# Optimization experiments

Measured on AMD Instinct MI355X. Metric: run time of the kernel, lower is better.

Reference implementation:

```python
import jax, jax.numpy as jnp
import numpy as np

ASSIGN_RATIO = 0.1  # hard-coded inside coarsen_graph in the original
EPS_CUT = 1e-7
EPS_NORM = 1e-12  # torch F.normalize eps


def _normalize_batch_adj(adj):
    # adj: [B, N, N]
    n = adj.shape[1]
    A = adj + jnp.eye(n, dtype=adj.dtype)
    deg_inv_sqrt = jnp.clip(A.sum(-1), 1.0, None) ** -0.5  # [B, N]
    newA = deg_inv_sqrt[..., :, None] * A * deg_inv_sqrt[..., None, :]
    row_mask = (adj.sum(-1) > 0).astype(adj.dtype)  # [B, N]
    return row_mask[..., :, None] * newA


def setup_inputs():
    key = jax.random.key(0)
    k0, k1, k2, k3, k4 = jax.random.split(key, 5)
    B, N, D, T = 512, 128, 256, 512
    concept_hidden = jax.random.normal(k0, (B, N, D), jnp.float32)
    adj = jax.random.uniform(k1, (B, N, N), jnp.float32)
    head = jax.random.randint(k2, (B, T), 0, N)
    lin_w = jax.random.normal(k3, (1, D), jnp.float32) / np.sqrt(D).astype(np.float32)
    bias = jax.random.normal(k4, (1,), jnp.float32)
    return {"concept_hidden": concept_hidden, "adj": adj, "head": head,
            "lin_w": lin_w, "bias": bias}


def reference(concept_hidden, adj, head, lin_w, bias):
    # concept_hidden: [B, N, D], adj: [B, N, N], head: [B, T] node indices
    x = concept_hidden
    B, N, D = x.shape

    out = x @ lin_w.T                      # [B, N, 1]  self.lin(x)
    norm_adj = _normalize_batch_adj(adj)   # [B, N, N]
    out = norm_adj @ out + bias            # [B, N, 1]
    alpha = jax.nn.sigmoid(out ** 2)[..., 0]  # [B, N]

    # batch_num_nodes[i] = len(set(head[i]))  -> count unique via sort
    hs = jnp.sort(head, axis=-1)
    n_uniq = 1 + (hs[:, 1:] != hs[:, :-1]).sum(-1)  # [B]

    # per-sample k = ceil(n * 0.1) + 1 (only when n > 1); cut = k-th largest alpha
    k = jnp.ceil(n_uniq.astype(jnp.float32) * ASSIGN_RATIO).astype(jnp.int32) + 1
    a_desc = jnp.sort(alpha, axis=-1)[:, ::-1]       # descending
    idx = jnp.clip(k - 1, 0, N - 1)
    cut = jnp.take_along_axis(a_desc, idx[:, None], axis=-1)[:, 0]
    cut = jnp.where(n_uniq > 1, cut, jnp.zeros_like(cut))  # [B]

    cut_alpha = jax.nn.relu(alpha + EPS_CUT - cut[:, None])  # [B, N]

    # S = norm_adj * cut_alpha broadcast over rows, then L1-normalize rows
    S = norm_adj * cut_alpha[:, None, :]
    S = S / jnp.clip(jnp.abs(S).sum(-1, keepdims=True), EPS_NORM, None)

    St = jnp.swapaxes(S, 1, 2)             # [B, N, N]
    embedding_tensor = St @ x              # S^T x   [B, N, D]
    new_adj = (St @ adj) @ S               # S^T A S [B, N, N]
    return embedding_tensor, new_adj
```

## Files before the change

kernel.cpp:

```cpp
#include <hip/hip_runtime.h>

#define Bsz 512
#define Nn  128
#define Dd  256
#define Tt  512

typedef __attribute__((ext_vector_type(8))) short short8;
typedef __attribute__((ext_vector_type(4))) float f32x4;

__device__ __forceinline__ ushort f2bf(float f) {
    union { float f; unsigned u; } v; v.f = f;
    unsigned r = v.u + 0x7fffu + ((v.u >> 16) & 1u);
    return (ushort)(r >> 16);
}
__device__ __forceinline__ unsigned pk2(float a, float b) {
    return (unsigned)f2bf(a) | ((unsigned)f2bf(b) << 16);
}
__device__ __forceinline__ float bf2f(ushort u) {
    union { unsigned u; float f; } v; v.u = (unsigned)u << 16; return v.f;
}

__global__ __launch_bounds__(1024, 8) void mega(
    const float* __restrict__ x, const float* __restrict__ adj,
    const int* __restrict__ head, const float* __restrict__ lin_w,
    const float* __restrict__ bias,
    float* __restrict__ emb, float* __restrict__ nadj)
{
    const int b = blockIdx.x, t = threadIdx.x;
    __shared__ __align__(16) ushort adjB[Nn][136];
    __shared__ __align__(16) ushort STl[Nn][136];
    __shared__ float ttS[Nn], disS[Nn], maskS[Nn], alphaS[Nn], uS[Nn], rowcS[Nn];
    __shared__ float partS[Nn][9];
    __shared__ float dotP[Nn][4];
    __shared__ int   flags[Nn];
    __shared__ int   nuniq;
    __shared__ float cutS;

    const float bias0 = bias[0];
    if (t < Nn) flags[t] = 0;
    if (t == 0) { nuniq = 0; cutS = 0.f; }

    const float* adjb = adj + (size_t)b * Nn * Nn;
#pragma unroll
    for (int i = 0; i < 4; ++i) {
        int f = t + 1024 * i;
        int rr = f >> 5, c = (f & 31) * 4;
        float4 v = *(const float4*)&adjb[(size_t)rr * Nn + c];
        uint2 w2; w2.x = pk2(v.x, v.y); w2.y = pk2(v.z, v.w);
        *(uint2*)&adjB[rr][c] = w2;
    }
    __syncthreads();

    if (t < Tt) { int h = head[(size_t)b * Tt + t]; flags[h] = 1; }

    if (t < 512) {
        const int dr = t >> 2, dh = t & 3;
        const float4* xr = (const float4*)(x + ((size_t)b * Nn + dr) * Dd + dh * 64);
        const float4* wr = (const float4*)(lin_w + dh * 64);
        float p = 0.f;
#pragma unroll
        for (int i = 0; i < 16; ++i) {
            float4 v = xr[i], w4 = wr[i];
            p += v.x * w4.x + v.y * w4.y + v.z * w4.z + v.w * w4.w;
        }
        dotP[dr][dh] = p;
    }

    const int r = t >> 3, seg = t & 7;
    {
        short8 a0 = *(const short8*)&adjB[r][seg * 16];
        short8 a1 = *(const short8*)&adjB[r][seg * 16 + 8];
        float s = 0.f;
#pragma unroll
        for (int j = 0; j < 8; ++j) s += bf2f((ushort)a0[j]) + bf2f((ushort)a1[j]);
        partS[r][seg] = s;
    }
    __syncthreads();

    if (t < Nn) {
        float rs = 0.f;
#pragma unroll
        for (int j = 0; j < 8; ++j) rs += partS[t][j];
        float dt = dotP[t][0] + dotP[t][1] + dotP[t][2] + dotP[t][3];
        maskS[t]  = (rs > 0.f) ? 1.f : 0.f;
        float dis = 1.f / sqrtf(fmaxf(rs + 1.f, 1.f));
        disS[t]   = dis;
        ttS[t]    = dis * dt;
        atomicAdd(&nuniq, flags[t]);
    }
    __syncthreads();

    {
        short8 a0 = *(const short8*)&adjB[r][seg * 16];
        short8 a1 = *(const short8*)&adjB[r][seg * 16 + 8];
        float s = 0.f;
#pragma unroll
        for (int j = 0; j < 8; ++j) {
            s += bf2f((ushort)a0[j]) * ttS[seg * 16 + j];
            s += bf2f((ushort)a1[j]) * ttS[seg * 16 + 8 + j];
        }
        partS[r][seg] = s;
    }
    __syncthreads();
    if (t < Nn) {
        float mv = 0.f;
#pragma unroll
        for (int j = 0; j < 8; ++j) mv += partS[t][j];
        float o = maskS[t] * disS[t] * (mv + ttS[t]) + bias0;
        alphaS[t] = 1.f / (1.f + expf(-o * o));
    }
    __syncthreads();
    if (t < Nn) {
        int nu = nuniq;
        if (nu > 1) {
            int idx = (int)ceilf((float)nu * 0.1f);
            if (idx > Nn - 1) idx = Nn - 1;
            float an = alphaS[t];
            int cg = 0, ce = 0;
            for (int j = 0; j < Nn; ++j) {
                float aj = alphaS[j];
                cg += (aj > an); ce += (aj == an);
            }
            if (cg <= idx && idx < cg + ce) cutS = an;
        }
    }
    __syncthreads();
    if (t < Nn) uS[t] = fmaxf(alphaS[t] + 1e-7f - cutS, 0.f) * disS[t];
    __syncthreads();
    {
        short8 a0 = *(const short8*)&adjB[r][seg * 16];
        short8 a1 = *(const short8*)&adjB[r][seg * 16 + 8];
        float s = 0.f;
#pragma unroll
        for (int j = 0; j < 8; ++j) {
            s += bf2f((ushort)a0[j]) * uS[seg * 16 + j];
            s += bf2f((ushort)a1[j]) * uS[seg * 16 + 8 + j];
        }
        partS[r][seg] = s;
    }
    __syncthreads();
    if (t < Nn) {
        float tot = uS[t];
#pragma unroll
        for (int j = 0; j < 8; ++j) tot += partS[t][j];
        float rsum = maskS[t] * disS[t] * tot;
        rowcS[t]   = maskS[t] * disS[t] / fmaxf(rsum, 1e-12f);
    }
    __syncthreads();

    {
        const int m = t & 127, sl = t >> 7, k0 = sl * 16;
        const float um = uS[m];
        float vv[16];
#pragma unroll
        for (int j = 0; j < 16; ++j) {
            int k = k0 + j;
            vv[j] = rowcS[k] * (bf2f(adjB[k][m]) + ((k == m) ? 1.f : 0.f)) * um;
        }
        uint4 p0, p1;
        p0.x = pk2(vv[0],  vv[1]);  p0.y = pk2(vv[2],  vv[3]);
        p0.z = pk2(vv[4],  vv[5]);  p0.w = pk2(vv[6],  vv[7]);
        p1.x = pk2(vv[8],  vv[9]);  p1.y = pk2(vv[10], vv[11]);
        p1.z = pk2(vv[12], vv[13]); p1.w = pk2(vv[14], vv[15]);
        *(uint4*)&STl[m][k0]     = p0;
        *(uint4*)&STl[m][k0 + 8] = p1;
    }
    __syncthreads();

    const int lane = t & 63, w = t >> 6;
    const int l15 = lane & 15, quad = lane >> 4;
    const int mrow  = (w & 7) * 16;
    const int nhalf = (w >> 3) * 64;
    f32x4 acc[4];

#pragma unroll
    for (int nt = 0; nt < 4; ++nt) acc[nt] = (f32x4){0.f, 0.f, 0.f, 0.f};
#pragma unroll
    for (int k0 = 0; k0 < 128; k0 += 32) {
        short8 a0 = *(const short8*)&adjB[mrow + l15][k0 + quad * 8];
#pragma unroll
        for (int nt = 0; nt < 4; ++nt) {
            short8 bf = *(const short8*)&STl[nhalf + nt * 16 + l15][k0 + quad * 8];
            acc[nt] = __builtin_amdgcn_mfma_f32_16x16x32_bf16(a0, bf, acc[nt], 0, 0, 0);
        }
    }
    __syncthreads();

    ushort (*PT)[136] = (ushort(*)[136])&adjB[0][0];
#pragma unroll
    for (int nt = 0; nt < 4; ++nt) {
        int j    = nhalf + nt * 16 + l15;
        int mcol = mrow + quad * 4;
        uint2 w2;
        w2.x = pk2(acc[nt][0], acc[nt][1]);
        w2.y = pk2(acc[nt][2], acc[nt][3]);
        *(uint2*)&PT[j][mcol] = w2;
    }
    __syncthreads();

#pragma unroll
    for (int nt = 0; nt < 4; ++nt) acc[nt] = (f32x4){0.f, 0.f, 0.f, 0.f};
#pragma unroll
    for (int k0 = 0; k0 < 128; k0 += 32) {
        short8 a0 = *(const short8*)&STl[mrow + l15][k0 + quad * 8];
#pragma unroll
        for (int nt = 0; nt < 4; ++nt) {
            short8 bf = *(const short8*)&PT[nhalf + nt * 16 + l15][k0 + quad * 8];
            acc[nt] = __builtin_amdgcn_mfma_f32_16x16x32_bf16(a0, bf, acc[nt], 0, 0, 0);
        }
    }
#pragma unroll
    for (int nt = 0; nt < 4; ++nt)
#pragma unroll
        for (int rr = 0; rr < 4; ++rr) {
            int row = mrow + quad * 4 + rr;
            int col = nhalf + nt * 16 + l15;
            nadj[((size_t)b * Nn + row) * Nn + col] = acc[nt][rr];
        }
    __syncthreads();

    uint (*xTp)[68] = (uint(*)[68])&adjB[0][0];
    short8 aE[4];
#pragma unroll
    for (int ks = 0; ks < 4; ++ks)
        aE[ks] = *(const short8*)&STl[mrow + l15][ks * 32 + quad * 8];
    const int dcb = (w >> 3) * 64;

    for (int half = 0; half < 2; ++half) {
        const int d0 = half * 128;
#pragma unroll
        for (int i = 0; i < 2; ++i) {
            int f = t + 1024 * i;
            int d4 = f & 31, kp = f >> 5;
            const float* xp = x + ((size_t)b * Nn + 2 * kp) * Dd + d0 + 4 * d4;
            float4 ve = *(const float4*)xp;
            float4 vo = *(const float4*)(xp + Dd);
            xTp[4 * d4    ][kp] = pk2(ve.x, vo.x);
            xTp[4 * d4 + 1][kp] = pk2(ve.y, vo.y);
            xTp[4 * d4 + 2][kp] = pk2(ve.z, vo.z);
            xTp[4 * d4 + 3][kp] = pk2(ve.w, vo.w);
        }
        __syncthreads();
        f32x4 accE[4];
#pragma unroll
        for (int nt = 0; nt < 4; ++nt) accE[nt] = (f32x4){0.f, 0.f, 0.f, 0.f};
#pragma unroll
        for (int ks = 0; ks < 4; ++ks) {
#pragma unroll
            for (int nt = 0; nt < 4; ++nt) {
                short8 bf = *(const short8*)&xTp[dcb + nt * 16 + l15][ks * 16 + quad * 4];
                accE[nt] = __builtin_amdgcn_mfma_f32_16x16x32_bf16(aE[ks], bf, accE[nt], 0, 0, 0);
            }
        }
#pragma unroll
        for (int nt = 0; nt < 4; ++nt)
#pragma unroll
            for (int rr = 0; rr < 4; ++rr) {
                int row = mrow + quad * 4 + rr;
                int col = d0 + dcb + nt * 16 + l15;
                emb[((size_t)b * Nn + row) * Dd + col] = accE[nt][rr];
            }
        __syncthreads();
    }
}

extern "C" void kernel_launch(void* const* d_in, const int* in_sizes, int n_in,
                              void* d_out, int out_size, void* d_ws, size_t ws_size,
                              hipStream_t stream)
{
    const float* x     = (const float*)d_in[0];
    const float* adj   = (const float*)d_in[1];
    const int*   head  = (const int*)d_in[2];
    const float* lin_w = (const float*)d_in[3];
    const float* bias  = (const float*)d_in[4];

    float* emb  = (float*)d_out;
    float* nadj = emb + (size_t)Bsz * Nn * Dd;

    mega<<<Bsz, 1024, 0, stream>>>(x, adj, head, lin_w, bias, emb, nadj);
}
```

Measured before the change: 199.7 us.

## Overlap adj load with dot products, shuffle reductions, prefetch x into registers

The first phase is split so half the threads compute the x·w dot products while the other half load and convert adj to bf16. The shared-memory partial-sum arrays and their extra barriers are replaced by wavefront shuffle reductions. The x tiles for the embedding GEMM are loaded into registers before the second adjacency GEMM and before the first embedding half, hiding global latency behind MFMA work. In exchange it uses more registers and issues strided scalar x loads instead of float4 loads.

After: 198.9 us. About the same (-0.4%).

```diff
diff --git a/kernel.cpp b/kernel.cpp
--- a/kernel.cpp
+++ b/kernel.cpp
@@ -30,8 +30,7 @@
     __shared__ __align__(16) ushort adjB[Nn][136];
     __shared__ __align__(16) ushort STl[Nn][136];
     __shared__ float ttS[Nn], disS[Nn], maskS[Nn], alphaS[Nn], uS[Nn], rowcS[Nn];
-    __shared__ float partS[Nn][9];
-    __shared__ float dotP[Nn][4];
+    __shared__ float dotL[Nn];
     __shared__ int   flags[Nn];
     __shared__ int   nuniq;
     __shared__ float cutS;
@@ -40,20 +39,9 @@
     if (t < Nn) flags[t] = 0;
     if (t == 0) { nuniq = 0; cutS = 0.f; }
 
-    const float* adjb = adj + (size_t)b * Nn * Nn;
-#pragma unroll
-    for (int i = 0; i < 4; ++i) {
-        int f = t + 1024 * i;
-        int rr = f >> 5, c = (f & 31) * 4;
-        float4 v = *(const float4*)&adjb[(size_t)rr * Nn + c];
-        uint2 w2; w2.x = pk2(v.x, v.y); w2.y = pk2(v.z, v.w);
-        *(uint2*)&adjB[rr][c] = w2;
-    }
-    __syncthreads();
-
-    if (t < Tt) { int h = head[(size_t)b * Tt + t]; flags[h] = 1; }
-
+    int hv = 0;
     if (t < 512) {
+        hv = head[(size_t)b * Tt + t];
         const int dr = t >> 2, dh = t & 3;
         const float4* xr = (const float4*)(x + ((size_t)b * Nn + dr) * Dd + dh * 64);
         const float4* wr = (const float4*)(lin_w + dh * 64);
@@ -63,8 +51,24 @@
             float4 v = xr[i], w4 = wr[i];
             p += v.x * w4.x + v.y * w4.y + v.z * w4.z + v.w * w4.w;
         }
-        dotP[dr][dh] = p;
-    }
+        p += __shfl_xor(p, 1, 64);
+        p += __shfl_xor(p, 2, 64);
+        if (dh == 0) dotL[dr] = p;
+    } else {
+        const int t2 = t - 512;
+        const float* adjb = adj + (size_t)b * Nn * Nn;
+#pragma unroll
+        for (int i = 0; i < 8; ++i) {
+            int f = t2 + 512 * i;
+            int rr = f >> 5, c = (f & 31) * 4;
+            float4 v = *(const float4*)&adjb[(size_t)rr * Nn + c];
+            uint2 w2; w2.x = pk2(v.x, v.y); w2.y = pk2(v.z, v.w);
+            *(uint2*)&adjB[rr][c] = w2;
+        }
+    }
+    __syncthreads();
+
+    if (t < Tt) flags[hv] = 1;
 
     const int r = t >> 3, seg = t & 7;
     {
@@ -73,20 +77,15 @@
         float s = 0.f;
 #pragma unroll
         for (int j = 0; j < 8; ++j) s += bf2f((ushort)a0[j]) + bf2f((ushort)a1[j]);
-        partS[r][seg] = s;
-    }
-    __syncthreads();
-
-    if (t < Nn) {
-        float rs = 0.f;
-#pragma unroll
-        for (int j = 0; j < 8; ++j) rs += partS[t][j];
-        float dt = dotP[t][0] + dotP[t][1] + dotP[t][2] + dotP[t][3];
-        maskS[t]  = (rs > 0.f) ? 1.f : 0.f;
-        float dis = 1.f / sqrtf(fmaxf(rs + 1.f, 1.f));
-        disS[t]   = dis;
-        ttS[t]    = dis * dt;
-        atomicAdd(&nuniq, flags[t]);
+        s += __shfl_xor(s, 1, 64);
+        s += __shfl_xor(s, 2, 64);
+        s += __shfl_xor(s, 4, 64);
+        if (seg == 0) {
+            maskS[r] = (s > 0.f) ? 1.f : 0.f;
+            float dis = 1.f / sqrtf(fmaxf(s + 1.f, 1.f));
+            disS[r] = dis;
+            ttS[r]  = dis * dotL[r];
+        }
     }
     __syncthreads();
 
@@ -99,17 +98,17 @@
             s += bf2f((ushort)a0[j]) * ttS[seg * 16 + j];
             s += bf2f((ushort)a1[j]) * ttS[seg * 16 + 8 + j];
         }
-        partS[r][seg] = s;
-    }
-    __syncthreads();
-    if (t < Nn) {
-        float mv = 0.f;
-#pragma unroll
-        for (int j = 0; j < 8; ++j) mv += partS[t][j];
-        float o = maskS[t] * disS[t] * (mv + ttS[t]) + bias0;
-        alphaS[t] = 1.f / (1.f + expf(-o * o));
-    }
-    __syncthreads();
+        s += __shfl_xor(s, 1, 64);
+        s += __shfl_xor(s, 2, 64);
+        s += __shfl_xor(s, 4, 64);
+        if (seg == 0) {
+            float o = maskS[r] * disS[r] * (s + ttS[r]) + bias0;
+            alphaS[r] = 1.f / (1.f + expf(-o * o));
+            atomicAdd(&nuniq, flags[r]);
+        }
+    }
+    __syncthreads();
+
     if (t < Nn) {
         int nu = nuniq;
         if (nu > 1) {
@@ -127,6 +126,7 @@
     __syncthreads();
     if (t < Nn) uS[t] = fmaxf(alphaS[t] + 1e-7f - cutS, 0.f) * disS[t];
     __syncthreads();
+
     {
         short8 a0 = *(const short8*)&adjB[r][seg * 16];
         short8 a1 = *(const short8*)&adjB[r][seg * 16 + 8];
@@ -136,15 +136,13 @@
             s += bf2f((ushort)a0[j]) * uS[seg * 16 + j];
             s += bf2f((ushort)a1[j]) * uS[seg * 16 + 8 + j];
         }
-        partS[r][seg] = s;
-    }
-    __syncthreads();
-    if (t < Nn) {
-        float tot = uS[t];
-#pragma unroll
-        for (int j = 0; j < 8; ++j) tot += partS[t][j];
-        float rsum = maskS[t] * disS[t] * tot;
-        rowcS[t]   = maskS[t] * disS[t] / fmaxf(rsum, 1e-12f);
+        s += __shfl_xor(s, 1, 64);
+        s += __shfl_xor(s, 2, 64);
+        s += __shfl_xor(s, 4, 64);
+        if (seg == 0) {
+            float rsum = maskS[r] * disS[r] * (uS[r] + s);
+            rowcS[r]   = maskS[r] * disS[r] / fmaxf(rsum, 1e-12f);
+        }
     }
     __syncthreads();
 
@@ -198,6 +196,16 @@
     }
     __syncthreads();
 
+    const int xrow = t & 127, kq0 = t >> 7;
+    float xv0[8], xv1[8];
+    {
+        const float* xb = x + (size_t)b * Nn * Dd + xrow;
+#pragma unroll
+        for (int k = 0; k < 8; ++k) xv0[k] = xb[(size_t)(8 * kq0 + k) * Dd];
+#pragma unroll
+        for (int k = 0; k < 8; ++k) xv1[k] = xb[(size_t)(8 * (kq0 + 8) + k) * Dd];
+    }
+
 #pragma unroll
     for (int nt = 0; nt < 4; ++nt) acc[nt] = (f32x4){0.f, 0.f, 0.f, 0.f};
 #pragma unroll
@@ -212,56 +220,87 @@
 #pragma unroll
     for (int nt = 0; nt < 4; ++nt)
 #pragma unroll
-        for (int rr = 0; rr < 4; ++rr) {
-            int row = mrow + quad * 4 + rr;
+        for (int rr2 = 0; rr2 < 4; ++rr2) {
+            int row = mrow + quad * 4 + rr2;
             int col = nhalf + nt * 16 + l15;
-            nadj[((size_t)b * Nn + row) * Nn + col] = acc[nt][rr];
+            nadj[((size_t)b * Nn + row) * Nn + col] = acc[nt][rr2];
         }
     __syncthreads();
 
     uint (*xTp)[68] = (uint(*)[68])&adjB[0][0];
-    short8 aE[4];
-#pragma unroll
-    for (int ks = 0; ks < 4; ++ks)
-        aE[ks] = *(const short8*)&STl[mrow + l15][ks * 32 + quad * 8];
     const int dcb = (w >> 3) * 64;
 
-    for (int half = 0; half < 2; ++half) {
-        const int d0 = half * 128;
-#pragma unroll
-        for (int i = 0; i < 2; ++i) {
-            int f = t + 1024 * i;
-            int d4 = f & 31, kp = f >> 5;
-            const float* xp = x + ((size_t)b * Nn + 2 * kp) * Dd + d0 + 4 * d4;
-            float4 ve = *(const float4*)xp;
-            float4 vo = *(const float4*)(xp + Dd);
-            xTp[4 * d4    ][kp] = pk2(ve.x, vo.x);
-            xTp[4 * d4 + 1][kp] = pk2(ve.y, vo.y);
-            xTp[4 * d4 + 2][kp] = pk2(ve.z, vo.z);
-            xTp[4 * d4 + 3][kp] = pk2(ve.w, vo.w);
-        }
-        __syncthreads();
-        f32x4 accE[4];
-#pragma unroll
-        for (int nt = 0; nt < 4; ++nt) accE[nt] = (f32x4){0.f, 0.f, 0.f, 0.f};
-#pragma unroll
-        for (int ks = 0; ks < 4; ++ks) {
-#pragma unroll
-            for (int nt = 0; nt < 4; ++nt) {
-                short8 bf = *(const short8*)&xTp[dcb + nt * 16 + l15][ks * 16 + quad * 4];
-                accE[nt] = __builtin_amdgcn_mfma_f32_16x16x32_bf16(aE[ks], bf, accE[nt], 0, 0, 0);
-            }
-        }
-#pragma unroll
-        for (int nt = 0; nt < 4; ++nt)
-#pragma unroll
-            for (int rr = 0; rr < 4; ++rr) {
-                int row = mrow + quad * 4 + rr;
-                int col = d0 + dcb + nt * 16 + l15;
-                emb[((size_t)b * Nn + row) * Dd + col] = accE[nt][rr];
-            }
-        __syncthreads();
-    }
+    {
+        uint4 q;
+        q.x = pk2(xv0[0], xv0[1]); q.y = pk2(xv0[2], xv0[3]);
+        q.z = pk2(xv0[4], xv0[5]); q.w = pk2(xv0[6], xv0[7]);
+        *(uint4*)&xTp[xrow][4 * kq0] = q;
+        q.x = pk2(xv1[0], xv1[1]); q.y = pk2(xv1[2], xv1[3]);
+        q.z = pk2(xv1[4], xv1[5]); q.w = pk2(xv1[6], xv1[7]);
+        *(uint4*)&xTp[xrow][4 * (kq0 + 8)] = q;
+    }
+    __syncthreads();
+
+    {
+        const float* xb = x + (size_t)b * Nn * Dd + 128 + xrow;
+#pragma unroll
+        for (int k = 0; k < 8; ++k) xv0[k] = xb[(size_t)(8 * kq0 + k) * Dd];
+#pragma unroll
+        for (int k = 0; k < 8; ++k) xv1[k] = xb[(size_t)(8 * (kq0 + 8) + k) * Dd];
+    }
+
+    f32x4 accE[4];
+#pragma unroll
+    for (int nt = 0; nt < 4; ++nt) accE[nt] = (f32x4){0.f, 0.f, 0.f, 0.f};
+#pragma unroll
+    for (int ks = 0; ks < 4; ++ks) {
+        short8 aE = *(const short8*)&STl[mrow + l15][ks * 32 + quad * 8];
+#pragma unroll
+        for (int nt = 0; nt < 4; ++nt) {
+            short8 bf = *(const short8*)&xTp[dcb + nt * 16 + l15][ks * 16 + quad * 4];
+            accE[nt] = __builtin_amdgcn_mfma_f32_16x16x32_bf16(aE, bf, accE[nt], 0, 0, 0);
+        }
+    }
+#pragma unroll
+    for (int nt = 0; nt < 4; ++nt)
+#pragma unroll
+        for (int rr2 = 0; rr2 < 4; ++rr2) {
+            int row = mrow + quad * 4 + rr2;
+            int col = dcb + nt * 16 + l15;
+            emb[((size_t)b * Nn + row) * Dd + col] = accE[nt][rr2];
+        }
+    __syncthreads();
+
+    {
+        uint4 q;
+        q.x = pk2(xv0[0], xv0[1]); q.y = pk2(xv0[2], xv0[3]);
+        q.z = pk2(xv0[4], xv0[5]); q.w = pk2(xv0[6], xv0[7]);
+        *(uint4*)&xTp[xrow][4 * kq0] = q;
+        q.x = pk2(xv1[0], xv1[1]); q.y = pk2(xv1[2], xv1[3]);
+        q.z = pk2(xv1[4], xv1[5]); q.w = pk2(xv1[6], xv1[7]);
+        *(uint4*)&xTp[xrow][4 * (kq0 + 8)] = q;
+    }
+    __syncthreads();
+
+#pragma unroll
+    for (int nt = 0; nt < 4; ++nt) accE[nt] = (f32x4){0.f, 0.f, 0.f, 0.f};
+#pragma unroll
+    for (int ks = 0; ks < 4; ++ks) {
+        short8 aE = *(const short8*)&STl[mrow + l15][ks * 32 + quad * 8];
+#pragma unroll
+        for (int nt = 0; nt < 4; ++nt) {
+            short8 bf = *(const short8*)&xTp[dcb + nt * 16 + l15][ks * 16 + quad * 4];
+            accE[nt] = __builtin_amdgcn_mfma_f32_16x16x32_bf16(aE, bf, accE[nt], 0, 0, 0);
+        }
+    }
+#pragma unroll
+    for (int nt = 0; nt < 4; ++nt)
+#pragma unroll
+        for (int rr2 = 0; rr2 < 4; ++rr2) {
+            int row = mrow + quad * 4 + rr2;
+            int col = 128 + dcb + nt * 16 + l15;
+            emb[((size_t)b * Nn + row) * Dd + col] = accE[nt][rr2];
+        }
 }
 
 extern "C" void kernel_launch(void* const* d_in, const int* in_sizes, int n_in,
```
